# Performance work log

Hardware: AMD Instinct MI355X
Metric: run time of the kernel (lower is better)

Reference implementation:

```python
import jax, jax.numpy as jnp
import numpy as np

K = 3       # kernel size
PAD = 1     # k // 2
S = 1       # stride
EPS = 1e-5  # BatchNorm eps


def setup_inputs() -> dict:
    key = jax.random.key(0)
    ks = jax.random.split(key, 7)
    B, C1, C2, H, W = 4, 256, 256, 80, 80
    x = jax.random.normal(ks[0], (B, C1, H, W), dtype=jnp.float32)
    # offset/mask conv params (orig inits these to zero; use small random so
    # the deformable sampling path is actually exercised)
    w_off = jax.random.normal(ks[1], (3 * K * K, C1, K, K), dtype=jnp.float32) * 0.01
    b_off = jax.random.normal(ks[2], (3 * K * K,), dtype=jnp.float32) * 0.01
    weight = jax.random.normal(ks[3], (C2, C1, K, K), dtype=jnp.float32) * 0.05
    bias = jax.random.normal(ks[4], (C2,), dtype=jnp.float32) * 0.05
    gamma = jnp.ones((C2,), dtype=jnp.float32)
    beta = jnp.zeros((C2,), dtype=jnp.float32)
    return {"x": x, "w_off": w_off, "b_off": b_off, "weight": weight,
            "bias": bias, "gamma": gamma, "beta": beta}


def _elastic_head(x, w_off, b_off, weight, bias, gamma, beta):
    B, C, H, W = x.shape
    K2 = K * K
    # offset/mask predictor conv (stride 1, SAME padding -> output H x W)
    off_out = jax.lax.conv_general_dilated(
        x, w_off, (S, S), 'SAME',
        dimension_numbers=('NCHW', 'OIHW', 'NCHW')) + b_off[None, :, None, None]
    o1, o2, m = off_out[:, :K2], off_out[:, K2:2 * K2], off_out[:, 2 * K2:]
    mask = jax.nn.sigmoid(m)                                   # [B,K2,H,W]
    # torchvision layout: channel 2p = dy_p, 2p+1 = dx_p
    off = jnp.concatenate([o1, o2], axis=1).reshape(B, K2, 2, H, W)
    dy, dx = off[:, :, 0], off[:, :, 1]                        # [B,K2,H,W]
    # base sampling grid per kernel tap
    ii, jj = jnp.meshgrid(jnp.arange(K), jnp.arange(K), indexing='ij')
    ii = ii.reshape(K2)
    jj = jj.reshape(K2)
    base_y = (jnp.arange(H)[None, :] * S - PAD + ii[:, None]).astype(x.dtype)  # [K2,H]
    base_x = (jnp.arange(W)[None, :] * S - PAD + jj[:, None]).astype(x.dtype)  # [K2,W]
    ys = dy + base_y[None, :, :, None]                         # [B,K2,H,W]
    xs = dx + base_x[None, :, None, :]
    y0 = jnp.floor(ys)
    x0 = jnp.floor(xs)
    wy = ys - y0
    wx = xs - x0
    y0i = y0.astype(jnp.int32)
    x0i = x0.astype(jnp.int32)
    y1i = y0i + 1
    x1i = x0i + 1
    x_flat = x.reshape(B, C, H * W)

    def gather(yy, xx):
        valid = ((yy >= 0) & (yy < H) & (xx >= 0) & (xx < W)).astype(x.dtype)
        idx = jnp.clip(yy, 0, H - 1) * W + jnp.clip(xx, 0, W - 1)
        g = jax.vmap(lambda xf, ix: xf[:, ix])(x_flat, idx.reshape(B, -1))
        return g.reshape(B, C, K2, H, W) * valid[:, None]

    # bilinear sample with zero padding outside, accumulate corners
    patches = (gather(y0i, x0i) * ((1 - wy) * (1 - wx))[:, None]
               + gather(y0i, x1i) * ((1 - wy) * wx)[:, None]
               + gather(y1i, x0i) * (wy * (1 - wx))[:, None]
               + gather(y1i, x1i) * (wy * wx)[:, None])       # [B,C,K2,H,W]
    patches = patches * mask[:, None]                          # modulation
    # implicit GEMM of deform_conv2d
    out = jnp.einsum('bcphw,ocp->bohw', patches,
                     weight.reshape(weight.shape[0], C, K2)) + bias[None, :, None, None]
    # BatchNorm2d (training-mode batch stats, biased variance) + SiLU
    mean = out.mean(axis=(0, 2, 3))
    var = out.var(axis=(0, 2, 3))
    xn = (out - mean[None, :, None, None]) * jax.lax.rsqrt(var + EPS)[None, :, None, None]
    y_bn = xn * gamma[None, :, None, None] + beta[None, :, None, None]
    return y_bn * jax.nn.sigmoid(y_bn)


def reference(x, w_off, b_off, weight, bias, gamma, beta):
    return _elastic_head(x, w_off, b_off, weight, bias, gamma, beta)
```

## Files before the change

kernel.cpp:

```cpp
#include <hip/hip_runtime.h>
#include <math.h>

constexpr int Hc = 80, Wc = 80, Bn = 4, C1 = 256, C2 = 256;
constexpr int HWn = Hc * Wc;
constexpr int NPIX = Bn * HWn;
constexpr int OFFC = 27;
constexpr int KK   = 2304;

typedef short bf16x8 __attribute__((ext_vector_type(8)));
typedef float f32x4  __attribute__((ext_vector_type(4)));

__device__ __forceinline__ unsigned f2bf(float f) {
    unsigned u = __float_as_uint(f);
    return (u + 0x7FFF + ((u >> 16) & 1)) >> 16;
}

__device__ __forceinline__ unsigned packhi2(float v0, float v1) {
    unsigned h;
    asm("v_cvt_pk_bf16_f32 %0, %1, %2" : "=v"(h) : "v"(v0), "v"(v1));
    return h;
}

__global__ __launch_bounds__(256) void k_wprep(const float* __restrict__ weight,
                                               unsigned short* __restrict__ wB1)
{
    int e = blockIdx.x * 256 + threadIdx.x;
    int kin = e & 7;
    int oc  = (e >> 3) & 255;
    int kg  = (e >> 11) & 3;
    int s   = e >> 13;
    int p   = s >> 3, cc = s & 7;
    float w = weight[((size_t)oc * C1 + cc * 32 + kg * 8 + kin) * 9 + p];
    wB1[e] = (unsigned short)f2bf(w);
}

__global__ __launch_bounds__(256) void k_wobprep(const float* __restrict__ w_off,
                                                 unsigned short* __restrict__ wOB)
{
    int e = blockIdx.x * 256 + threadIdx.x;
    int k  = e & 31;
    int oc = (e >> 5) & 31;
    int s  = e >> 10;
    int p  = s >> 3, cc = s & 7;
    float v = 0.f;
    if (oc < 27) v = w_off[((size_t)oc * C1 + cc * 32 + k) * 9 + p];
    wOB[e] = (unsigned short)f2bf(v);
}

__global__ __launch_bounds__(256) void k_xtrans(const float* __restrict__ x,
                                                float* __restrict__ xT,
                                                unsigned short* __restrict__ xTb)
{
    __shared__ float tile[32][33];
    int bid = blockIdx.x;
    int ct  = bid & 7;
    int hwt = (bid >> 3) % 200;
    int b   = bid / 1600;
    int c0  = ct * 32, hw0 = hwt * 32;
    int tid = threadIdx.x;
    int col = tid & 31, rw = tid >> 5;
    const float* xb = x + (size_t)b * C1 * HWn;
    #pragma unroll
    for (int k = 0; k < 4; ++k) {
        int r = rw + k * 8;
        tile[r][col] = xb[(size_t)(c0 + r) * HWn + hw0 + col];
    }
    __syncthreads();
    float* xo = xT + ((size_t)b * HWn + hw0) * C1 + c0;
    unsigned short* xob = xTb + ((size_t)b * HWn + hw0) * C1 + c0;
    #pragma unroll
    for (int k = 0; k < 4; ++k) {
        int r = rw + k * 8;
        float v = tile[col][r];
        xo[(size_t)r * C1 + col]  = v;
        xob[(size_t)r * C1 + col] = (unsigned short)f2bf(v);
    }
}

__global__ __launch_bounds__(256) void k_offmfma(const unsigned short* __restrict__ xTb,
                                                 const unsigned short* __restrict__ wOB,
                                                 const float* __restrict__ b_off,
                                                 float* __restrict__ off)
{
    int t  = threadIdx.x;
    int wv = t >> 6, lane = t & 63;
    int li = lane & 15, kg = lane >> 4;
    int mi = wv & 1;
    int nj = wv >> 1;

    int mtile = ((blockIdx.x & 7) * 100) + (blockIdx.x >> 3);
    int m0  = mtile * 32;
    int b   = m0 / HWn;
    int hw0 = m0 - b * HWn;
    int pxl = hw0 + mi * 16 + li;
    int h = pxl / Wc, w = pxl - h * Wc;

    const unsigned short* xb = xTb + (size_t)b * HWn * C1;

    f32x4 acc = (f32x4){0.f, 0.f, 0.f, 0.f};
    #pragma unroll
    for (int p = 0; p < 9; ++p) {
        int dh = p / 3 - 1, dw = p % 3 - 1;
        int hh = h + dh, ww = w + dw;
        bool valid = (hh >= 0 && hh < Hc && ww >= 0 && ww < Wc);
        int hwp = valid ? (hh * Wc + ww) : 0;
        const unsigned short* arow = xb + (size_t)hwp * C1 + kg * 8;
        const unsigned short* brow = wOB + ((size_t)(p * 8) * 32 + nj * 16 + li) * 32 + kg * 8;
        #pragma unroll
        for (int cc = 0; cc < 8; ++cc) {
            uint4 av = *(const uint4*)(arow + cc * 32);
            if (!valid) av = make_uint4(0, 0, 0, 0);
            uint4 bv = *(const uint4*)(brow + cc * 1024);
            acc = __builtin_amdgcn_mfma_f32_16x16x32_bf16(
                __builtin_bit_cast(bf16x8, av), __builtin_bit_cast(bf16x8, bv), acc, 0, 0, 0);
        }
    }
    int oc = nj * 16 + li;
    if (oc < OFFC) {
        float bs = b_off[oc];
        float4 v;
        v.x = acc[0] + bs; v.y = acc[1] + bs; v.z = acc[2] + bs; v.w = acc[3] + bs;
        int hwd = hw0 + mi * 16 + kg * 4;
        *(float4*)&off[((size_t)b * OFFC + oc) * HWn + hwd] = v;
    }
}

__global__ __launch_bounds__(256) void k_meta(const float* __restrict__ off,
                                              int* __restrict__ crdbuf,
                                              float4* __restrict__ w4buf)
{
    int pair = blockIdx.x * 256 + threadIdx.x;
    int px = pair / 9, p = pair - px * 9;
    int b  = px / HWn, hw = px - b * HWn;
    int h = hw / Wc, w = hw - h * Wc;
    int ii = p / 3, jj = p - ii * 3;

    const float* ob = off + (size_t)b * OFFC * HWn + hw;
    float dy = ob[(2 * p) * HWn];
    float dx = ob[(2 * p + 1) * HWn];
    float mv = ob[(18 + p) * HWn];
    float mask = 1.0f / (1.0f + expf(-mv));
    float ys = dy + (float)(h - 1 + ii);
    float xsv = dx + (float)(w - 1 + jj);
    float y0f = floorf(ys), x0f = floorf(xsv);
    float wy = ys - y0f, wx = xsv - x0f;
    int y0 = (int)y0f, x0 = (int)x0f;
    int y1 = y0 + 1, x1 = x0 + 1;
    float vy0 = (y0 >= 0 && y0 < Hc) ? 1.f : 0.f;
    float vy1 = (y1 >= 0 && y1 < Hc) ? 1.f : 0.f;
    float vx0 = (x0 >= 0 && x0 < Wc) ? 1.f : 0.f;
    float vx1 = (x1 >= 0 && x1 < Wc) ? 1.f : 0.f;
    float4 wv;
    wv.x = mask * (1.f - wy) * (1.f - wx) * vy0 * vx0;
    wv.y = mask * (1.f - wy) * wx         * vy0 * vx1;
    wv.z = mask * wy         * (1.f - wx) * vy1 * vx0;
    wv.w = mask * wy         * wx         * vy1 * vx1;
    int cy0 = min(max(y0, 0), Hc - 1), cy1 = min(max(y1, 0), Hc - 1);
    int cx0 = min(max(x0, 0), Wc - 1), cx1 = min(max(x1, 0), Wc - 1);
    crdbuf[pair] = cy0 | (cy1 << 8) | (cx0 << 16) | (cx1 << 24);
    w4buf[pair]  = wv;
}

__global__ __launch_bounds__(256) void k_gather(const float* __restrict__ xT,
                                                const int* __restrict__ crdbuf,
                                                const float4* __restrict__ w4buf,
                                                unsigned short* __restrict__ Ahi)
{
    int t   = threadIdx.x;
    int wv  = t >> 6, l = t & 63;
    int xcd = blockIdx.x & 7;
    int blk = blockIdx.x >> 3;
    int wgl = (xcd * 100 + blk) * 4 + wv;
    int base = wgl * 72;

    #pragma unroll 2
    for (int i = 0; i < 72; ++i) {
        int pair = base + i;
        int px = pair / 9, p = pair - px * 9;
        int b  = px / HWn;
        int crd = crdbuf[pair];
        float4 w4 = w4buf[pair];
        int cy0 = crd & 255, cy1 = (crd >> 8) & 255;
        int cx0 = (crd >> 16) & 255, cx1 = (crd >> 24) & 255;
        const float* xt = xT + (size_t)b * HWn * C1;
        const float4* g00p = (const float4*)&xt[(size_t)(cy0 * Wc + cx0) * C1];
        const float4* g01p = (const float4*)&xt[(size_t)(cy0 * Wc + cx1) * C1];
        const float4* g10p = (const float4*)&xt[(size_t)(cy1 * Wc + cx0) * C1];
        const float4* g11p = (const float4*)&xt[(size_t)(cy1 * Wc + cx1) * C1];
        float4 g00 = g00p[l], g01 = g01p[l], g10 = g10p[l], g11 = g11p[l];
        float vx = fmaf(w4.x, g00.x, fmaf(w4.y, g01.x, fmaf(w4.z, g10.x, w4.w * g11.x)));
        float vy = fmaf(w4.x, g00.y, fmaf(w4.y, g01.y, fmaf(w4.z, g10.y, w4.w * g11.y)));
        float vz = fmaf(w4.x, g00.z, fmaf(w4.y, g01.z, fmaf(w4.z, g10.z, w4.w * g11.z)));
        float vw = fmaf(w4.x, g00.w, fmaf(w4.y, g01.w, fmaf(w4.z, g10.w, w4.w * g11.w)));
        unsigned h0 = packhi2(vx, vy), h1 = packhi2(vz, vw);
        int s = p * 8 + (l >> 3);
        size_t aidx = ((size_t)s * NPIX + px) * 32 + 4 * (l & 7);
        *(uint2*)&Ahi[aidx] = make_uint2(h0, h1);
    }
}

__global__ __launch_bounds__(256, 4) void k_dmfma(const unsigned short* __restrict__ Ahi,
                                                  const unsigned short* __restrict__ wB1,
                                                  const float* __restrict__ bias,
                                                  float* __restrict__ out)
{
    __shared__ __align__(16) char smem[32768];
    float* Tb = (float*)smem;

    int t  = threadIdx.x;
    int wv = t >> 6, lane = t & 63;
    int li = lane & 15, kg = lane >> 4;
    int nh = wv;

    int mtile = ((blockIdx.x & 7) * 100) + (blockIdx.x >> 3);
    int m0  = mtile * 32;
    int b   = m0 / HWn;
    int hw0 = m0 - b * HWn;
    int row0 = m0 + li;
    int row1 = m0 + 16 + li;

    auto gllB = [&](int s, int buf) {
        const char* src = (const char*)wB1 + (size_t)s * 16384 + t * 16;
        char* dst = smem + buf * 16384 + t * 16;
        #pragma unroll
        for (int i = 0; i < 4; ++i)
            __builtin_amdgcn_global_load_lds(
                (const __attribute__((address_space(1))) void*)(src + i * 4096),
                (__attribute__((address_space(3))) void*)(dst + i * 4096),
                16, 0, 0);
    };
    auto loadA = [&](int s, uint4& h0, uint4& h1) {
        size_t base = (size_t)s * NPIX * 32 + (size_t)kg * 8;
        h0 = *(const uint4*)(Ahi + base + (size_t)row0 * 32);
        h1 = *(const uint4*)(Ahi + base + (size_t)row1 * 32);
    };

    f32x4 acc[2][4];
    #pragma unroll
    for (int m = 0; m < 2; ++m)
        #pragma unroll
        for (int n = 0; n < 4; ++n) acc[m][n] = (f32x4){0.f, 0.f, 0.f, 0.f};

    uint4 a0m0, a0m1, a1m0, a1m1, a2m0, a2m1;
    loadA(0, a0m0, a0m1);
    gllB(0, 0);
    loadA(1, a1m0, a1m1);

    auto step = [&](int s, uint4& c0, uint4& c1, uint4& l0, uint4& l1) {
        if (s == 71) { asm volatile("s_waitcnt vmcnt(0)" ::: "memory"); }
        else         { asm volatile("s_waitcnt vmcnt(2)" ::: "memory"); }
        __builtin_amdgcn_s_barrier();
        __builtin_amdgcn_sched_barrier(0);
        int cur = s & 1;
        if (s < 71) gllB(s + 1, cur ^ 1);
        __builtin_amdgcn_sched_barrier(0);
        if (s < 70) loadA(s + 2, l0, l1);
        __builtin_amdgcn_sched_barrier(0);
        const unsigned short* Bc = (const unsigned short*)(smem + cur * 16384);
        bf16x8 a0 = __builtin_bit_cast(bf16x8, c0);
        bf16x8 a1 = __builtin_bit_cast(bf16x8, c1);
        __builtin_amdgcn_s_setprio(1);
        #pragma unroll
        for (int nt = 0; nt < 4; ++nt) {
            bf16x8 bv = *(const bf16x8*)&Bc[(kg * 256 + nh * 64 + nt * 16 + li) * 8];
            acc[0][nt] = __builtin_amdgcn_mfma_f32_16x16x32_bf16(a0, bv, acc[0][nt], 0, 0, 0);
            acc[1][nt] = __builtin_amdgcn_mfma_f32_16x16x32_bf16(a1, bv, acc[1][nt], 0, 0, 0);
        }
        __builtin_amdgcn_s_setprio(0);
    };

    for (int s = 0; s < 72; s += 3) {
        step(s,     a0m0, a0m1, a2m0, a2m1);
        step(s + 1, a1m0, a1m1, a0m0, a0m1);
        step(s + 2, a2m0, a2m1, a1m0, a1m1);
    }

    #pragma unroll
    for (int q = 0; q < 8; ++q) {
        __syncthreads();
        if (nh == (q >> 1)) {
            #pragma unroll
            for (int jj = 0; jj < 2; ++jj) {
                int nt = (q & 1) * 2 + jj;
                #pragma unroll
                for (int m = 0; m < 2; ++m) {
                    f32x4 a = acc[m][nt];
                    int rrw = jj * 16 + li;
                    int col = m * 16 + kg * 4;
                    #pragma unroll
                    for (int r = 0; r < 4; ++r)
                        Tb[rrw * 33 + col + r] = a[r];
                }
            }
        }
        __syncthreads();
        int px = t & 31;
        int rw = t >> 5;
        #pragma unroll
        for (int it = 0; it < 4; ++it) {
            int r  = it * 8 + rw;
            int oc = q * 32 + r;
            out[(size_t)(b * C2 + oc) * HWn + hw0 + px] = Tb[r * 33 + px] + bias[oc];
        }
    }
}

__global__ __launch_bounds__(256) void k_bnstats(const float* __restrict__ out,
                                                 float* __restrict__ stats)
{
    int oc = blockIdx.x;
    double s = 0.0, ss = 0.0;
    for (int i = threadIdx.x; i < NPIX; i += 256) {
        int bb = i / HWn;
        int hw = i - bb * HWn;
        float v = out[(size_t)(bb * C2 + oc) * HWn + hw];
        s  += (double)v;
        ss += (double)v * (double)v;
    }
    __shared__ double ls[256], lss[256];
    ls[threadIdx.x] = s; lss[threadIdx.x] = ss;
    __syncthreads();
    for (int st = 128; st > 0; st >>= 1) {
        if (threadIdx.x < st) {
            ls[threadIdx.x]  += ls[threadIdx.x + st];
            lss[threadIdx.x] += lss[threadIdx.x + st];
        }
        __syncthreads();
    }
    if (threadIdx.x == 0) {
        double mean = ls[0] / (double)NPIX;
        double var  = lss[0] / (double)NPIX - mean * mean;
        stats[oc]       = (float)mean;
        stats[256 + oc] = (float)(1.0 / sqrt(var + 1e-5));
    }
}

__global__ __launch_bounds__(256) void k_bnsilu(float* __restrict__ out,
                                                const float* __restrict__ stats,
                                                const float* __restrict__ gamma,
                                                const float* __restrict__ beta)
{
    int n4 = (Bn * C2 * HWn) / 4;
    for (int i = blockIdx.x * blockDim.x + threadIdx.x; i < n4;
         i += gridDim.x * blockDim.x) {
        float4 v = ((float4*)out)[i];
        int e  = i * 4;
        int oc = (e / HWn) & 255;
        float mean = stats[oc];
        float gs   = gamma[oc] * stats[256 + oc];
        float bt   = beta[oc];
        float y;
        y = (v.x - mean) * gs + bt; v.x = y / (1.f + expf(-y));
        y = (v.y - mean) * gs + bt; v.y = y / (1.f + expf(-y));
        y = (v.z - mean) * gs + bt; v.z = y / (1.f + expf(-y));
        y = (v.w - mean) * gs + bt; v.w = y / (1.f + expf(-y));
        ((float4*)out)[i] = v;
    }
}

extern "C" void kernel_launch(void* const* d_in, const int* in_sizes, int n_in,
                              void* d_out, int out_size, void* d_ws, size_t ws_size,
                              hipStream_t stream)
{
    const float* x      = (const float*)d_in[0];
    const float* w_off  = (const float*)d_in[1];
    const float* b_off  = (const float*)d_in[2];
    const float* weight = (const float*)d_in[3];
    const float* bias   = (const float*)d_in[4];
    const float* gamma  = (const float*)d_in[5];
    const float* beta   = (const float*)d_in[6];
    float* out = (float*)d_out;

    char* wsb = (char*)d_ws;
    unsigned short* Ahi  = (unsigned short*)(wsb);
    float*          xT   = (float*)(wsb + 117964800);
    unsigned short* xTb  = (unsigned short*)(wsb + 144179200);
    float*          off  = (float*)(wsb + 157286400);
    unsigned short* wB1  = (unsigned short*)(wsb + 160051200);
    unsigned short* wOB  = (unsigned short*)(wsb + 161230848);
    int*            crdb = (int*)(wsb + 161378304);
    float4*         w4b  = (float4*)(wsb + 162299904);
    float*         stats = (float*)(wsb + 165986304);

    k_wprep    <<<2304, 256, 0, stream>>>(weight, wB1);
    k_wobprep  <<<288, 256, 0, stream>>>(w_off, wOB);
    k_xtrans   <<<6400, 256, 0, stream>>>(x, xT, xTb);
    k_offmfma  <<<800, 256, 0, stream>>>(xTb, wOB, b_off, off);
    k_meta     <<<900, 256, 0, stream>>>(off, crdb, w4b);
    k_gather   <<<800, 256, 0, stream>>>(xT, crdb, w4b, Ahi);
    k_dmfma    <<<800, 256, 0, stream>>>(Ahi, wB1, bias, out);
    k_bnstats  <<<256, 256, 0, stream>>>(out, stats);
    k_bnsilu   <<<2048, 256, 0, stream>>>(out, stats, gamma, beta);
}
```

Before: 253.0 us.

## Load GEMM B operand directly from global into registers, drop LDS staging

The MFMA GEMM kernel no longer stages weight tiles in LDS through global_load_lds with double buffering and per-step barriers. Each wave now loads its own B fragments straight from global memory into registers, with a two-stage register double buffer for both A and B. This removes the per-step barriers and LDS traffic and shrinks shared memory to the transpose buffer, which may raise occupancy. In exchange, B fragments are loaded redundantly by every block through L2/L1 and use more registers, with no explicit waitcnt control.

New measurement: 250.3 us. Within noise of the previous version (-1.1%).

```diff
diff --git a/kernel.cpp b/kernel.cpp
--- a/kernel.cpp
+++ b/kernel.cpp
@@ -204,8 +204,7 @@
                                                   const float* __restrict__ bias,
                                                   float* __restrict__ out)
 {
-    __shared__ __align__(16) char smem[32768];
-    float* Tb = (float*)smem;
+    __shared__ float Tb[32 * 33];
 
     int t  = threadIdx.x;
     int wv = t >> 6, lane = t & 63;
@@ -219,20 +218,21 @@
     int row0 = m0 + li;
     int row1 = m0 + 16 + li;
 
-    auto gllB = [&](int s, int buf) {
-        const char* src = (const char*)wB1 + (size_t)s * 16384 + t * 16;
-        char* dst = smem + buf * 16384 + t * 16;
-        #pragma unroll
-        for (int i = 0; i < 4; ++i)
-            __builtin_amdgcn_global_load_lds(
-                (const __attribute__((address_space(1))) void*)(src + i * 4096),
-                (__attribute__((address_space(3))) void*)(dst + i * 4096),
-                16, 0, 0);
+    const unsigned short* a0p = Ahi + (size_t)row0 * 32 + kg * 8;
+    const unsigned short* a1p = Ahi + (size_t)row1 * 32 + kg * 8;
+    const unsigned short* bp  = wB1 + (size_t)(kg * 256 + nh * 64 + li) * 8;
+
+    auto loadA = [&](int s, uint4& h0, uint4& h1) {
+        size_t o = (size_t)s * NPIX * 32;
+        h0 = *(const uint4*)(a0p + o);
+        h1 = *(const uint4*)(a1p + o);
     };
-    auto loadA = [&](int s, uint4& h0, uint4& h1) {
-        size_t base = (size_t)s * NPIX * 32 + (size_t)kg * 8;
-        h0 = *(const uint4*)(Ahi + base + (size_t)row0 * 32);
-        h1 = *(const uint4*)(Ahi + base + (size_t)row1 * 32);
+    auto loadB = [&](int s, uint4& b0, uint4& b1, uint4& b2, uint4& b3) {
+        const unsigned short* q = bp + (size_t)s * 8192;
+        b0 = *(const uint4*)(q);
+        b1 = *(const uint4*)(q + 128);
+        b2 = *(const uint4*)(q + 256);
+        b3 = *(const uint4*)(q + 384);
     };
 
     f32x4 acc[2][4];
@@ -241,38 +241,35 @@
         #pragma unroll
         for (int n = 0; n < 4; ++n) acc[m][n] = (f32x4){0.f, 0.f, 0.f, 0.f};
 
-    uint4 a0m0, a0m1, a1m0, a1m1, a2m0, a2m1;
-    loadA(0, a0m0, a0m1);
-    gllB(0, 0);
-    loadA(1, a1m0, a1m1);
-
-    auto step = [&](int s, uint4& c0, uint4& c1, uint4& l0, uint4& l1) {
-        if (s == 71) { asm volatile("s_waitcnt vmcnt(0)" ::: "memory"); }
-        else         { asm volatile("s_waitcnt vmcnt(2)" ::: "memory"); }
-        __builtin_amdgcn_s_barrier();
-        __builtin_amdgcn_sched_barrier(0);
-        int cur = s & 1;
-        if (s < 71) gllB(s + 1, cur ^ 1);
-        __builtin_amdgcn_sched_barrier(0);
-        if (s < 70) loadA(s + 2, l0, l1);
-        __builtin_amdgcn_sched_barrier(0);
-        const unsigned short* Bc = (const unsigned short*)(smem + cur * 16384);
+    uint4 aA0, aA1, bA0, bA1, bA2, bA3;
+    uint4 aB0, aB1, bB0, bB1, bB2, bB3;
+
+    auto compute = [&](uint4& c0, uint4& c1, uint4& q0, uint4& q1, uint4& q2, uint4& q3) {
         bf16x8 a0 = __builtin_bit_cast(bf16x8, c0);
         bf16x8 a1 = __builtin_bit_cast(bf16x8, c1);
         __builtin_amdgcn_s_setprio(1);
-        #pragma unroll
-        for (int nt = 0; nt < 4; ++nt) {
-            bf16x8 bv = *(const bf16x8*)&Bc[(kg * 256 + nh * 64 + nt * 16 + li) * 8];
-            acc[0][nt] = __builtin_amdgcn_mfma_f32_16x16x32_bf16(a0, bv, acc[0][nt], 0, 0, 0);
-            acc[1][nt] = __builtin_amdgcn_mfma_f32_16x16x32_bf16(a1, bv, acc[1][nt], 0, 0, 0);
-        }
+        bf16x8 v;
+        v = __builtin_bit_cast(bf16x8, q0);
+        acc[0][0] = __builtin_amdgcn_mfma_f32_16x16x32_bf16(a0, v, acc[0][0], 0, 0, 0);
+        acc[1][0] = __builtin_amdgcn_mfma_f32_16x16x32_bf16(a1, v, acc[1][0], 0, 0, 0);
+        v = __builtin_bit_cast(bf16x8, q1);
+        acc[0][1] = __builtin_amdgcn_mfma_f32_16x16x32_bf16(a0, v, acc[0][1], 0, 0, 0);
+        acc[1][1] = __builtin_amdgcn_mfma_f32_16x16x32_bf16(a1, v, acc[1][1], 0, 0, 0);
+        v = __builtin_bit_cast(bf16x8, q2);
+        acc[0][2] = __builtin_amdgcn_mfma_f32_16x16x32_bf16(a0, v, acc[0][2], 0, 0, 0);
+        acc[1][2] = __builtin_amdgcn_mfma_f32_16x16x32_bf16(a1, v, acc[1][2], 0, 0, 0);
+        v = __builtin_bit_cast(bf16x8, q3);
+        acc[0][3] = __builtin_amdgcn_mfma_f32_16x16x32_bf16(a0, v, acc[0][3], 0, 0, 0);
+        acc[1][3] = __builtin_amdgcn_mfma_f32_16x16x32_bf16(a1, v, acc[1][3], 0, 0, 0);
         __builtin_amdgcn_s_setprio(0);
     };
 
-    for (int s = 0; s < 72; s += 3) {
-        step(s,     a0m0, a0m1, a2m0, a2m1);
-        step(s + 1, a1m0, a1m1, a0m0, a0m1);
-        step(s + 2, a2m0, a2m1, a1m0, a1m1);
+    loadA(0, aA0, aA1); loadB(0, bA0, bA1, bA2, bA3);
+    for (int s = 0; s < 72; s += 2) {
+        loadA(s + 1, aB0, aB1); loadB(s + 1, bB0, bB1, bB2, bB3);
+        compute(aA0, aA1, bA0, bA1, bA2, bA3);
+        if (s + 2 < 72) { loadA(s + 2, aA0, aA1); loadB(s + 2, bA0, bA1, bA2, bA3); }
+        compute(aB0, aB1, bB0, bB1, bB2, bB3);
     }
 
     #pragma unroll
```
